# Kernel optimization log

Measured on AMD Instinct MI355X. Metric: run time of the kernel, lower is better.

The kernel has to match this reference:

```python
import jax, jax.numpy as jnp
import numpy as np


def setup_inputs() -> dict:
    key = jax.random.key(0)
    k1, k2 = jax.random.split(key)
    img = jax.random.normal(k1, (8, 64, 256, 256), dtype=jnp.float32)
    # normalized grid coordinates in [-1, 1]
    points = jax.random.uniform(k2, (8, 384, 384, 2), dtype=jnp.float32,
                                minval=-1.0, maxval=1.0)
    return {"img": img, "points": points}


def reference(img, points):
    """Faithful port of mmcv bilinear_grid_sample(im, grid, align_corners=False)."""
    n, c, h, w = img.shape
    gn, gh, gw, _ = points.shape
    x = points[..., 0].reshape(n, -1)  # (n, P)
    y = points[..., 1].reshape(n, -1)

    # unnormalize (align_corners=False)
    x = ((x + 1.0) * w - 1.0) / 2.0
    y = ((y + 1.0) * h - 1.0) / 2.0

    x0 = jnp.floor(x)
    y0 = jnp.floor(y)
    x1 = x0 + 1.0
    y1 = y0 + 1.0

    # bilinear weights computed from UNCLAMPED coords (matches mmcv)
    wa = ((x1 - x) * (y1 - y))[:, None, :]  # (n, 1, P)
    wb = ((x1 - x) * (y - y0))[:, None, :]
    wc = ((x - x0) * (y1 - y))[:, None, :]
    wd = ((x - x0) * (y - y0))[:, None, :]

    # zero-pad by 1 on each spatial side, shift indices by +1, clamp into pad
    im_p = jnp.pad(img, ((0, 0), (0, 0), (1, 1), (1, 1)))
    ph, pw = h + 2, w + 2
    x0i = jnp.clip(x0.astype(jnp.int32) + 1, 0, pw - 1)
    x1i = jnp.clip(x1.astype(jnp.int32) + 1, 0, pw - 1)
    y0i = jnp.clip(y0.astype(jnp.int32) + 1, 0, ph - 1)
    y1i = jnp.clip(y1.astype(jnp.int32) + 1, 0, ph - 1)

    im_flat = im_p.reshape(n, c, ph * pw)
    P = x0i.shape[-1]

    def gather(yi, xi):
        idx = (yi * pw + xi)[:, None, :]  # (n, 1, P)
        return jnp.take_along_axis(im_flat, jnp.broadcast_to(idx, (n, c, P)), axis=2)

    Ia = gather(y0i, x0i)
    Ib = gather(y1i, x0i)
    Ic = gather(y0i, x1i)
    Id = gather(y1i, x1i)

    out = Ia * wa + Ib * wb + Ic * wc + Id * wd  # (n, c, P)
    return out.reshape(n, c, gh, gw)
```

## Files before the change

### kernel.cpp

```cpp
#include <hip/hip_runtime.h>


#define NN 8
#define CC 64
#define HH 256
#define WW 256
#define HWSZ (HH * WW)
#define PP (384 * 384)
#define CHUNKS (PP / 64)
#define NQ (NN * 2)

__device__ __forceinline__ unsigned int bf16rne(float f) {
    unsigned int u = __float_as_uint(f);
    return (u + 0x7FFFu + ((u >> 16) & 1u)) >> 16;
}

__global__ __launch_bounds__(256) void repack_kernel(
    const float* __restrict__ img, unsigned int* __restrict__ ws)
{
    const int hw = blockIdx.x * 256 + threadIdx.x;
    const int n  = blockIdx.y;
    const float* src = img + (size_t)n * CC * HWSZ + hw;

    unsigned int buf[CC / 2];
    #pragma unroll
    for (int c2 = 0; c2 < CC / 2; ++c2) {
        float f0 = src[(size_t)(2 * c2) * HWSZ];
        float f1 = src[(size_t)(2 * c2 + 1) * HWSZ];
        buf[c2] = bf16rne(f0) | (bf16rne(f1) << 16);
    }
    #pragma unroll
    for (int cg = 0; cg < 2; ++cg) {
        uint4* dst = (uint4*)(ws + ((size_t)(n * 2 + cg) * HWSZ + hw) * 16);
        #pragma unroll
        for (int k = 0; k < 4; ++k)
            dst[k] = make_uint4(buf[cg * 16 + 4 * k],     buf[cg * 16 + 4 * k + 1],
                                buf[cg * 16 + 4 * k + 2], buf[cg * 16 + 4 * k + 3]);
    }
}

__global__ __launch_bounds__(256) void sample_cl_kernel(
    const unsigned int* __restrict__ ws,
    const float* __restrict__ points,
    float* __restrict__ out)
{
    const int bid  = blockIdx.x;
    const int xcd  = bid & 7;
    const int seq  = bid >> 3;
    const int q    = xcd + 8 * (seq / CHUNKS);
    const int chunk = seq % CHUNKS;
    const int n  = q >> 1;
    const int cg = q & 1;
    const int qt = threadIdx.x & 3;
    const int p  = chunk * 64 + (threadIdx.x >> 2);

    float2 pt = ((const float2*)points)[(size_t)n * PP + p];
    float x = ((pt.x + 1.0f) * (float)WW - 1.0f) * 0.5f;
    float y = ((pt.y + 1.0f) * (float)HH - 1.0f) * 0.5f;

    float x0f = floorf(x);
    float y0f = floorf(y);
    float fx = x - x0f;
    float fy = y - y0f;
    int x0 = (int)x0f;
    int y0 = (int)y0f;
    int x1 = x0 + 1;
    int y1 = y0 + 1;

    bool vx0 = (x0 >= 0) && (x0 < WW);
    bool vx1 = (x1 >= 0) && (x1 < WW);
    bool vy0 = (y0 >= 0) && (y0 < HH);
    bool vy1 = (y1 >= 0) && (y1 < HH);

    float wa = (1.0f - fx) * (1.0f - fy);
    float wb = (1.0f - fx) * fy;
    float wc = fx * (1.0f - fy);
    float wd = fx * fy;

    wa = (vx0 && vy0) ? wa : 0.0f;
    wb = (vx0 && vy1) ? wb : 0.0f;
    wc = (vx1 && vy0) ? wc : 0.0f;
    wd = (vx1 && vy1) ? wd : 0.0f;

    int cx0 = min(max(x0, 0), WW - 1);
    int cx1 = min(max(x1, 0), WW - 1);
    int cy0 = min(max(y0, 0), HH - 1);
    int cy1 = min(max(y1, 0), HH - 1);

    const uint4* base = (const uint4*)ws + (size_t)q * (HWSZ * 4) + qt;
    const uint4* pa = base + (size_t)(cy0 * WW + cx0) * 4;
    const uint4* pb = base + (size_t)(cy1 * WW + cx0) * 4;
    const uint4* pc = base + (size_t)(cy0 * WW + cx1) * 4;
    const uint4* pd = base + (size_t)(cy1 * WW + cx1) * 4;

    uint4 A = *pa;
    uint4 B = *pb;
    uint4 C = *pc;
    uint4 D = *pd;

    float* outp = out + ((size_t)(n * CC) + cg * 32 + qt * 8) * PP + p;

    const unsigned int aw[4] = {A.x, A.y, A.z, A.w};
    const unsigned int bw[4] = {B.x, B.y, B.z, B.w};
    const unsigned int cw[4] = {C.x, C.y, C.z, C.w};
    const unsigned int dw[4] = {D.x, D.y, D.z, D.w};
    #pragma unroll
    for (int j = 0; j < 4; ++j) {
        float a0 = __uint_as_float(aw[j] << 16);
        float a1 = __uint_as_float(aw[j] & 0xFFFF0000u);
        float b0 = __uint_as_float(bw[j] << 16);
        float b1 = __uint_as_float(bw[j] & 0xFFFF0000u);
        float c0 = __uint_as_float(cw[j] << 16);
        float c1 = __uint_as_float(cw[j] & 0xFFFF0000u);
        float d0 = __uint_as_float(dw[j] << 16);
        float d1 = __uint_as_float(dw[j] & 0xFFFF0000u);
        float v0 = a0 * wa + b0 * wb + c0 * wc + d0 * wd;
        float v1 = a1 * wa + b1 * wb + c1 * wc + d1 * wd;
        __builtin_nontemporal_store(v0, outp + (size_t)(2 * j) * PP);
        __builtin_nontemporal_store(v1, outp + (size_t)(2 * j + 1) * PP);
    }
}

__global__ __launch_bounds__(256) void grid_sample_fallback(
    const float* __restrict__ img,
    const float* __restrict__ points,
    float* __restrict__ out)
{
    const int p  = blockIdx.x * 256 + threadIdx.x;
    const int c0 = blockIdx.y * 2;
    const int n  = blockIdx.z;

    float2 pt = ((const float2*)points)[(size_t)n * PP + p];
    float x = ((pt.x + 1.0f) * (float)WW - 1.0f) * 0.5f;
    float y = ((pt.y + 1.0f) * (float)HH - 1.0f) * 0.5f;
    float x0f = floorf(x), y0f = floorf(y);
    float fx = x - x0f, fy = y - y0f;
    int x0 = (int)x0f, y0 = (int)y0f, x1 = x0 + 1, y1 = y0 + 1;
    bool vx0 = (x0 >= 0) && (x0 < WW), vx1 = (x1 >= 0) && (x1 < WW);
    bool vy0 = (y0 >= 0) && (y0 < HH), vy1 = (y1 >= 0) && (y1 < HH);
    float wa = (1.0f - fx) * (1.0f - fy), wb = (1.0f - fx) * fy;
    float wc = fx * (1.0f - fy), wd = fx * fy;
    wa = (vx0 && vy0) ? wa : 0.0f;
    wb = (vx0 && vy1) ? wb : 0.0f;
    wc = (vx1 && vy0) ? wc : 0.0f;
    wd = (vx1 && vy1) ? wd : 0.0f;
    int cx0 = min(max(x0, 0), WW - 1), cx1 = min(max(x1, 0), WW - 1);
    int cy0 = min(max(y0, 0), HH - 1), cy1 = min(max(y1, 0), HH - 1);
    int ia = cy0 * WW + cx0, ib = cy1 * WW + cx0;
    int ic = cy0 * WW + cx1, id = cy1 * WW + cx1;
    const float* plane = img + ((size_t)(n * CC + c0)) * HWSZ;
    float* outp = out + ((size_t)(n * CC + c0)) * PP + p;
    #pragma unroll
    for (int k = 0; k < 2; ++k) {
        float v = plane[ia] * wa + plane[ib] * wb + plane[ic] * wc + plane[id] * wd;
        __builtin_nontemporal_store(v, outp);
        plane += HWSZ;
        outp  += PP;
    }
}

extern "C" void kernel_launch(void* const* d_in, const int* in_sizes, int n_in,
                              void* d_out, int out_size, void* d_ws, size_t ws_size,
                              hipStream_t stream) {
    const float* img = (const float*)d_in[0];
    const float* points = (const float*)d_in[1];
    float* out = (float*)d_out;

    const size_t ws_needed = (size_t)NN * HWSZ * CC * 2;
    if (ws_size >= ws_needed) {
        unsigned int* ws = (unsigned int*)d_ws;
        dim3 g1(HWSZ / 256, NN);
        repack_kernel<<<g1, 256, 0, stream>>>(img, ws);
        dim3 g2(NQ * CHUNKS);
        sample_cl_kernel<<<g2, 256, 0, stream>>>(ws, points, out);
    } else {
        dim3 g(PP / 256, CC / 2, NN);
        grid_sample_fallback<<<g, 256, 0, stream>>>(img, points, out);
    }
}
```

Measured before the change: 130.8 us.

## Stage sampled outputs through LDS for vectorized stores and remap repack to XCDs

```diff
diff --git a/kernel.cpp b/kernel.cpp
--- a/kernel.cpp
+++ b/kernel.cpp
@@ -9,6 +9,10 @@
 #define PP (384 * 384)
 #define CHUNKS (PP / 64)
 #define NQ (NN * 2)
+#define PCHUNKS (HWSZ / 64)
+#define LDSW 66
+
+typedef float f32x4 __attribute__((ext_vector_type(4)));
 
 __device__ __forceinline__ unsigned int bf16rne(float f) {
     unsigned int u = __float_as_uint(f);
@@ -18,25 +22,26 @@
 __global__ __launch_bounds__(256) void repack_kernel(
     const float* __restrict__ img, unsigned int* __restrict__ ws)
 {
-    const int hw = blockIdx.x * 256 + threadIdx.x;
-    const int n  = blockIdx.y;
-    const float* src = img + (size_t)n * CC * HWSZ + hw;
+    const int bid = blockIdx.x;
+    const int xcd = bid & 7;
+    const int seq = bid >> 3;
+    const int q   = xcd + 8 * (seq / PCHUNKS);
+    const int hw0 = (seq % PCHUNKS) * 64;
+    const int n   = q >> 1;
+    const int cg  = q & 1;
+    const int qt  = threadIdx.x & 3;
+    const int hw  = hw0 + (threadIdx.x >> 2);
 
-    unsigned int buf[CC / 2];
+    const float* src = img + ((size_t)(n * CC + cg * 32 + qt * 8)) * HWSZ + hw;
+    unsigned int buf[4];
     #pragma unroll
-    for (int c2 = 0; c2 < CC / 2; ++c2) {
-        float f0 = src[(size_t)(2 * c2) * HWSZ];
-        float f1 = src[(size_t)(2 * c2 + 1) * HWSZ];
-        buf[c2] = bf16rne(f0) | (bf16rne(f1) << 16);
+    for (int k = 0; k < 4; ++k) {
+        float f0 = src[(size_t)(2 * k) * HWSZ];
+        float f1 = src[(size_t)(2 * k + 1) * HWSZ];
+        buf[k] = bf16rne(f0) | (bf16rne(f1) << 16);
     }
-    #pragma unroll
-    for (int cg = 0; cg < 2; ++cg) {
-        uint4* dst = (uint4*)(ws + ((size_t)(n * 2 + cg) * HWSZ + hw) * 16);
-        #pragma unroll
-        for (int k = 0; k < 4; ++k)
-            dst[k] = make_uint4(buf[cg * 16 + 4 * k],     buf[cg * 16 + 4 * k + 1],
-                                buf[cg * 16 + 4 * k + 2], buf[cg * 16 + 4 * k + 3]);
-    }
+    uint4* dst = (uint4*)ws + ((size_t)q * HWSZ + hw) * 4 + qt;
+    *dst = make_uint4(buf[0], buf[1], buf[2], buf[3]);
 }
 
 __global__ __launch_bounds__(256) void sample_cl_kernel(
@@ -44,6 +49,8 @@
     const float* __restrict__ points,
     float* __restrict__ out)
 {
+    __shared__ float lds[32 * LDSW];
+
     const int bid  = blockIdx.x;
     const int xcd  = bid & 7;
     const int seq  = bid >> 3;
@@ -52,7 +59,8 @@
     const int n  = q >> 1;
     const int cg = q & 1;
     const int qt = threadIdx.x & 3;
-    const int p  = chunk * 64 + (threadIdx.x >> 2);
+    const int pl = threadIdx.x >> 2;
+    const int p  = chunk * 64 + pl;
 
     float2 pt = ((const float2*)points)[(size_t)n * PP + p];
     float x = ((pt.x + 1.0f) * (float)WW - 1.0f) * 0.5f;
@@ -88,17 +96,10 @@
     int cy1 = min(max(y1, 0), HH - 1);
 
     const uint4* base = (const uint4*)ws + (size_t)q * (HWSZ * 4) + qt;
-    const uint4* pa = base + (size_t)(cy0 * WW + cx0) * 4;
-    const uint4* pb = base + (size_t)(cy1 * WW + cx0) * 4;
-    const uint4* pc = base + (size_t)(cy0 * WW + cx1) * 4;
-    const uint4* pd = base + (size_t)(cy1 * WW + cx1) * 4;
-
-    uint4 A = *pa;
-    uint4 B = *pb;
-    uint4 C = *pc;
-    uint4 D = *pd;
-
-    float* outp = out + ((size_t)(n * CC) + cg * 32 + qt * 8) * PP + p;
+    uint4 A = base[(size_t)(cy0 * WW + cx0) * 4];
+    uint4 B = base[(size_t)(cy1 * WW + cx0) * 4];
+    uint4 C = base[(size_t)(cy0 * WW + cx1) * 4];
+    uint4 D = base[(size_t)(cy1 * WW + cx1) * 4];
 
     const unsigned int aw[4] = {A.x, A.y, A.z, A.w};
     const unsigned int bw[4] = {B.x, B.y, B.z, B.w};
@@ -116,9 +117,20 @@
         float d1 = __uint_as_float(dw[j] & 0xFFFF0000u);
         float v0 = a0 * wa + b0 * wb + c0 * wc + d0 * wd;
         float v1 = a1 * wa + b1 * wb + c1 * wc + d1 * wd;
-        __builtin_nontemporal_store(v0, outp + (size_t)(2 * j) * PP);
-        __builtin_nontemporal_store(v1, outp + (size_t)(2 * j + 1) * PP);
+        lds[(qt * 8 + 2 * j)     * LDSW + pl] = v0;
+        lds[(qt * 8 + 2 * j + 1) * LDSW + pl] = v1;
     }
+
+    __syncthreads();
+
+    const int r  = threadIdx.x >> 3;
+    const int c8 = (threadIdx.x & 7) * 8;
+    const float* srcl = &lds[r * LDSW + c8];
+    f32x4 f0 = {srcl[0], srcl[1], srcl[2], srcl[3]};
+    f32x4 f1 = {srcl[4], srcl[5], srcl[6], srcl[7]};
+    float* op = out + ((size_t)(n * CC) + cg * 32 + r) * PP + chunk * 64 + c8;
+    __builtin_nontemporal_store(f0, (f32x4*)op);
+    __builtin_nontemporal_store(f1, (f32x4*)(op + 4));
 }
 
 __global__ __launch_bounds__(256) void grid_sample_fallback(
@@ -169,10 +181,8 @@
     const size_t ws_needed = (size_t)NN * HWSZ * CC * 2;
     if (ws_size >= ws_needed) {
         unsigned int* ws = (unsigned int*)d_ws;
-        dim3 g1(HWSZ / 256, NN);
-        repack_kernel<<<g1, 256, 0, stream>>>(img, ws);
-        dim3 g2(NQ * CHUNKS);
-        sample_cl_kernel<<<g2, 256, 0, stream>>>(ws, points, out);
+        repack_kernel<<<NQ * PCHUNKS, 256, 0, stream>>>(img, ws);
+        sample_cl_kernel<<<NQ * CHUNKS, 256, 0, stream>>>(ws, points, out);
     } else {
         dim3 g(PP / 256, CC / 2, NN);
         grid_sample_fallback<<<g, 256, 0, stream>>>(img, points, out);
```

Measured after the change: 192.2 us. +47.0%, slower.
